# Optimization experiments

Hardware: AMD Instinct MI355X
Metric: run time of the kernel (lower is better)

The kernel has to match this reference:

```python
import jax, jax.numpy as jnp
import numpy as np

N, E, G = 100000, 1600000, 128
IN, HID, HEADS, EDIM, OUT = 16, 32, 4, 8, 4
HC = HEADS * HID


def _p(k, shape):
    return jax.random.normal(k, shape, jnp.float32) * 0.1


def setup_inputs():
    key = jax.random.key(0)
    ks = list(jax.random.split(key, 24))
    nxt = iter(ks)
    d = dict(
        x=jax.random.normal(next(nxt), (N, IN), jnp.float32),
        edge_index=jax.random.randint(next(nxt), (2, E), 0, N),
        edge_attr=jax.random.normal(next(nxt), (E, EDIM), jnp.float32),
        batch=jnp.sort(jax.random.randint(next(nxt), (N,), 0, G)),
    )
    # conv1: in=IN -> heads*hid
    d['wl1'] = _p(next(nxt), (IN, HC));  d['bl1'] = jnp.zeros((HC,), jnp.float32)
    d['wr1'] = _p(next(nxt), (IN, HC));  d['br1'] = jnp.zeros((HC,), jnp.float32)
    d['we1'] = _p(next(nxt), (EDIM, HC)); d['att1'] = _p(next(nxt), (HEADS, HID)); d['bc1'] = jnp.zeros((HC,), jnp.float32)
    # conv2: in=HC -> heads*hid
    d['wl2'] = _p(next(nxt), (HC, HC));  d['bl2'] = jnp.zeros((HC,), jnp.float32)
    d['wr2'] = _p(next(nxt), (HC, HC));  d['br2'] = jnp.zeros((HC,), jnp.float32)
    d['we2'] = _p(next(nxt), (EDIM, HC)); d['att2'] = _p(next(nxt), (HEADS, HID)); d['bc2'] = jnp.zeros((HC,), jnp.float32)
    # conv3: in=HC -> 1*hid (heads=1)
    d['wl3'] = _p(next(nxt), (HC, HID)); d['bl3'] = jnp.zeros((HID,), jnp.float32)
    d['wr3'] = _p(next(nxt), (HC, HID)); d['br3'] = jnp.zeros((HID,), jnp.float32)
    d['we3'] = _p(next(nxt), (EDIM, HID)); d['att3'] = _p(next(nxt), (1, HID)); d['bc3'] = jnp.zeros((HID,), jnp.float32)
    d['w_fc1'] = _p(next(nxt), (HID, 2 * HID)); d['b_fc1'] = jnp.zeros((2 * HID,), jnp.float32)
    d['w_fc2'] = _p(next(nxt), (2 * HID, OUT)); d['b_fc2'] = jnp.zeros((OUT,), jnp.float32)
    return d


def _gatv2(x, src, dst, eattr, wl, bl, wr, br, we, att, bias, n):
    # PyG GATv2Conv: e_ij = a^T . leaky_relu(Wl x_j + Wr x_i + We e_ij)
    H, C = att.shape
    xl = (x @ wl + bl).reshape(-1, H, C)  # source transform [N,H,C]
    xr = (x @ wr + br).reshape(-1, H, C)  # target transform [N,H,C]
    ea = (eattr @ we).reshape(-1, H, C)   # edge transform   [E,H,C]
    e = jax.nn.leaky_relu(xl[src] + xr[dst] + ea, 0.2)  # [E,H,C]
    logit = jnp.einsum('ehc,hc->eh', e, att)            # [E,H]
    m = jax.ops.segment_max(logit, dst, num_segments=n)
    p = jnp.exp(logit - m[dst])
    s = jax.ops.segment_sum(p, dst, num_segments=n)
    alpha = p / (s[dst] + 1e-16)                        # segment softmax per dst
    out = jax.ops.segment_sum(xl[src] * alpha[:, :, None], dst, num_segments=n)
    return out.reshape(n, H * C) + bias


def reference(x, edge_index, edge_attr, batch,
              wl1, bl1, wr1, br1, we1, att1, bc1,
              wl2, bl2, wr2, br2, we2, att2, bc2,
              wl3, bl3, wr3, br3, we3, att3, bc3,
              w_fc1, b_fc1, w_fc2, b_fc2):
    n = x.shape[0]
    src, dst = edge_index[0], edge_index[1]
    # add_self_loops=True with fill_value='mean' (mean of incoming edge_attr per node)
    ones_e = jnp.ones((src.shape[0],), x.dtype)
    cnt = jax.ops.segment_sum(ones_e, dst, num_segments=n)
    loop_attr = jax.ops.segment_sum(edge_attr, dst, num_segments=n) / jnp.maximum(cnt, 1.0)[:, None]
    ar = jnp.arange(n)
    src_a = jnp.concatenate([src, ar])
    dst_a = jnp.concatenate([dst, ar])
    ea = jnp.concatenate([edge_attr, loop_attr], axis=0)

    h = jax.nn.elu(_gatv2(x, src_a, dst_a, ea, wl1, bl1, wr1, br1, we1, att1, bc1, n))
    h = jax.nn.elu(_gatv2(h, src_a, dst_a, ea, wl2, bl2, wr2, br2, we2, att2, bc2, n))
    h = jax.nn.elu(_gatv2(h, src_a, dst_a, ea, wl3, bl3, wr3, br3, we3, att3, bc3, n))

    # global mean pool over graphs
    gs = jax.ops.segment_sum(h, batch, num_segments=G)
    gc = jax.ops.segment_sum(jnp.ones((n,), h.dtype), batch, num_segments=G)
    g = gs / jnp.maximum(gc, 1.0)[:, None]

    g = jax.nn.elu(g @ w_fc1 + b_fc1)
    return g @ w_fc2 + b_fc2
```

## Files before the change

### kernel.cpp

```cpp
#include <hip/hip_runtime.h>
#include <cstdint>
#include <type_traits>

constexpr int GNUM = 128;

typedef _Float16 h2 __attribute__((ext_vector_type(2)));
typedef _Float16 h4 __attribute__((ext_vector_type(4)));
typedef _Float16 h8 __attribute__((ext_vector_type(8)));
typedef float f4 __attribute__((ext_vector_type(4)));


__global__ __launch_bounds__(256) void hist_kernel(const int* __restrict__ dst,
                                                   int* __restrict__ cnt, int E) {
  int i = blockIdx.x * 256 + threadIdx.x;
  if (i < E) atomicAdd(&cnt[dst[i]], 1);
}

__global__ __launch_bounds__(256) void scan_part_kernel(const int* __restrict__ cnt,
                                                        int* __restrict__ bpart, int n) {
  __shared__ int red[256];
  int base = blockIdx.x * 512;
  int t = threadIdx.x;
  int s = 0;
  int i0 = base + t, i1 = base + 256 + t;
  if (i0 < n) s += cnt[i0] + 1;
  if (i1 < n) s += cnt[i1] + 1;
  red[t] = s;
  __syncthreads();
  for (int off = 128; off > 0; off >>= 1) {
    if (t < off) red[t] += red[t + off];
    __syncthreads();
  }
  if (t == 0) bpart[blockIdx.x] = red[0];
}

__global__ __launch_bounds__(1024) void scan_top_kernel(const int* __restrict__ bpart,
                                                        int* __restrict__ boff,
                                                        int* __restrict__ row_ptr,
                                                        int B, int n) {
  __shared__ int buf[1024];
  int t = threadIdx.x;
  buf[t] = (t < B) ? bpart[t] : 0;
  __syncthreads();
  for (int off = 1; off < 1024; off <<= 1) {
    int v = (t >= off) ? buf[t - off] : 0;
    __syncthreads();
    buf[t] += v;
    __syncthreads();
  }
  if (t < B) boff[t] = (t == 0) ? 0 : buf[t - 1];
  if (t == 0) row_ptr[n] = buf[1023];
}

__global__ __launch_bounds__(256) void scan_write_kernel(const int* __restrict__ cnt,
                                                         const int* __restrict__ boff,
                                                         int* __restrict__ row_ptr,
                                                         int* __restrict__ fill, int n) {
  __shared__ int red[256];
  int base = blockIdx.x * 512;
  int t = threadIdx.x;
  int i0 = base + 2 * t, i1 = base + 2 * t + 1;
  int v0 = (i0 < n) ? cnt[i0] + 1 : 0;
  int v1 = (i1 < n) ? cnt[i1] + 1 : 0;
  int val = v0 + v1;
  red[t] = val;
  __syncthreads();
  for (int off = 1; off < 256; off <<= 1) {
    int u = (t >= off) ? red[t - off] : 0;
    __syncthreads();
    red[t] += u;
    __syncthreads();
  }
  int o = boff[blockIdx.x] + red[t] - val;
  if (i0 < n) { row_ptr[i0] = o; fill[i0] = o; }
  if (i1 < n) { row_ptr[i1] = o + v0; fill[i1] = o + v0; }
}

__global__ __launch_bounds__(256) void scatter_kernel(const int* __restrict__ src,
                                                      const int* __restrict__ dst,
                                                      const float* __restrict__ ea,
                                                      int* __restrict__ fill,
                                                      int* __restrict__ csr_src,
                                                      _Float16* __restrict__ ea_csr, int E) {
  int i = blockIdx.x * 256 + threadIdx.x;
  if (i >= E) return;
  int d = dst[i];
  int p = atomicAdd(&fill[d], 1);
  csr_src[p] = src[i];
  float4 e0 = *(const float4*)&ea[(size_t)i * 8];
  float4 e1 = *(const float4*)&ea[(size_t)i * 8 + 4];
  h8 v;
  v[0] = (_Float16)e0.x; v[1] = (_Float16)e0.y; v[2] = (_Float16)e0.z; v[3] = (_Float16)e0.w;
  v[4] = (_Float16)e1.x; v[5] = (_Float16)e1.y; v[6] = (_Float16)e1.z; v[7] = (_Float16)e1.w;
  *(h8*)&ea_csr[(size_t)p * 8] = v;
}

__global__ __launch_bounds__(256) void selfloop_kernel(const int* __restrict__ row_ptr,
                                                       int* __restrict__ csr_src,
                                                       _Float16* __restrict__ ea_csr, int n) {
  int idx = blockIdx.x * 256 + threadIdx.x;
  int i = idx >> 3, c = idx & 7;
  if (i >= n) return;
  int s = row_ptr[i], e = row_ptr[i + 1] - 1;
  float a = 0.f;
  for (int j = s; j < e; j++) a += (float)ea_csr[(size_t)j * 8 + c];
  float inv = 1.f / fmaxf((float)(e - s), 1.f);
  ea_csr[(size_t)e * 8 + c] = (_Float16)(a * inv);
  if (c == 0) csr_src[e] = i;
}

__global__ __launch_bounds__(256) void pack_kernel(const float* __restrict__ w0,
                                                   _Float16* __restrict__ wp0,
                                                   const float* __restrict__ w1,
                                                   _Float16* __restrict__ wp1,
                                                   int Kreal, int Kpad, int NC) {
  const float* w = blockIdx.y ? w1 : w0;
  _Float16* wp = blockIdx.y ? wp1 : wp0;
  int KB = Kpad / 32;
  int total = (NC / 16) * KB * 64;
  int idx = blockIdx.x * 256 + threadIdx.x;
  if (idx >= total) return;
  int lane = idx & 63;
  int blk = idx >> 6;
  int nt = blk / KB, kb = blk % KB;
  int col = nt * 16 + (lane & 15);
  int krow = kb * 32 + (lane >> 4) * 8;
  h8 v;
#pragma unroll
  for (int j = 0; j < 8; j++)
    v[j] = (krow + j < Kreal) ? (_Float16)w[(size_t)(krow + j) * NC + col] : (_Float16)0.f;
  *(h8*)&wp[(size_t)idx * 8] = v;
}

__global__ __launch_bounds__(256) void cvt16_kernel(const float* __restrict__ x,
                                                    _Float16* __restrict__ x16, int total4) {
  int i = blockIdx.x * 256 + threadIdx.x;
  if (i >= total4) return;
  float4 v = ((const float4*)x)[i];
  h4 o;
  o[0] = (_Float16)v.x; o[1] = (_Float16)v.y; o[2] = (_Float16)v.z; o[3] = (_Float16)v.w;
  ((h4*)x16)[i] = o;
}


template <int K, int NCOLS>
__global__ __launch_bounds__(256) void k1m_kernel(const _Float16* __restrict__ x,
                                                  const _Float16* __restrict__ wp0,
                                                  const float* __restrict__ b0,
                                                  _Float16* __restrict__ out0,
                                                  const _Float16* __restrict__ wp1,
                                                  const float* __restrict__ b1,
                                                  _Float16* __restrict__ out1, int n) {
  constexpr int NT = NCOLS / 16, KB = K / 32;
  const _Float16* wp = blockIdx.y ? wp1 : wp0;
  const float* b = blockIdx.y ? b1 : b0;
  _Float16* out = blockIdx.y ? out1 : out0;

  int tid = threadIdx.x;
  int wave = tid >> 6, lane = tid & 63;
  int m = lane & 15, quad = lane >> 4;
  int node0 = blockIdx.x * 64 + wave * 16;

  h8 afrag[KB];
  int anode = node0 + m;
  if (anode < n) {
#pragma unroll
    for (int kb = 0; kb < KB; kb++)
      afrag[kb] = *(const h8*)&x[(size_t)anode * K + kb * 32 + quad * 8];
  } else {
#pragma unroll
    for (int kb = 0; kb < KB; kb++) afrag[kb] = (h8)(_Float16)0.f;
  }

  f4 acc[NT] = {};
#pragma unroll
  for (int nt = 0; nt < NT; nt++) {
#pragma unroll
    for (int kb = 0; kb < KB; kb++) {
      h8 bfrag = *(const h8*)&wp[((size_t)(nt * KB + kb) * 64 + lane) * 8];
      acc[nt] = __builtin_amdgcn_mfma_f32_16x16x32_f16(afrag[kb], bfrag, acc[nt], 0, 0, 0);
    }
  }

#pragma unroll
  for (int nt = 0; nt < NT; nt++) {
#pragma unroll
    for (int r = 0; r < 4; r++) {
      int row = node0 + quad * 4 + r;
      if (row < n) {
        int col = nt * 16 + m;
        out[(size_t)row * NCOLS + col] = (_Float16)(acc[nt][r] + b[col]);
      }
    }
  }
}

template <int NCOLS>
__global__ __launch_bounds__(256) void k1m16_kernel(const _Float16* __restrict__ x16,
                                                    const _Float16* __restrict__ wp0,
                                                    const float* __restrict__ b0,
                                                    _Float16* __restrict__ out0,
                                                    const _Float16* __restrict__ wp1,
                                                    const float* __restrict__ b1,
                                                    _Float16* __restrict__ out1, int n) {
  constexpr int NT = NCOLS / 16;
  const _Float16* wp = blockIdx.y ? wp1 : wp0;
  const float* b = blockIdx.y ? b1 : b0;
  _Float16* out = blockIdx.y ? out1 : out0;

  int tid = threadIdx.x;
  int wave = tid >> 6, lane = tid & 63;
  int m = lane & 15, quad = lane >> 4;
  int node0 = blockIdx.x * 64 + wave * 16;

  int anode = node0 + m;
  h8 afrag;
  if (anode < n && quad < 2)
    afrag = *(const h8*)&x16[(size_t)anode * 16 + quad * 8];
  else
    afrag = (h8)(_Float16)0.f;

  f4 acc[NT] = {};
#pragma unroll
  for (int nt = 0; nt < NT; nt++) {
    h8 bfrag = *(const h8*)&wp[((size_t)nt * 64 + lane) * 8];
    acc[nt] = __builtin_amdgcn_mfma_f32_16x16x32_f16(afrag, bfrag, acc[nt], 0, 0, 0);
  }

#pragma unroll
  for (int nt = 0; nt < NT; nt++) {
#pragma unroll
    for (int r = 0; r < 4; r++) {
      int row = node0 + quad * 4 + r;
      if (row < n) {
        int col = nt * 16 + m;
        out[(size_t)row * NCOLS + col] = (_Float16)(acc[nt][r] + b[col]);
      }
    }
  }
}

template <int H>
__global__ __launch_bounds__(128) void k2_kernel(
    const _Float16* __restrict__ xl, const _Float16* __restrict__ xr,
    const int* __restrict__ row_ptr, const int* __restrict__ csr_src,
    const _Float16* __restrict__ ea_csr, const float* __restrict__ we,
    const float* __restrict__ att, const float* __restrict__ bc,
    _Float16* __restrict__ out, int n) {
  constexpr int HC = H * 32;
  constexpr int NL = HC / 4;
  constexpr int NPB = 128 / NL;

  int tid = threadIdx.x;
  int ln = tid / NL, q = tid % NL;
  int c0 = 4 * q;
  int node = blockIdx.x * NPB + ln;
  if (node >= n) return;

  h2 w2[8][2];
#pragma unroll
  for (int k = 0; k < 8; k++) {
    float4 v = *(const float4*)&we[k * HC + c0];
    w2[k][0] = h2{(_Float16)v.x, (_Float16)v.y};
    w2[k][1] = h2{(_Float16)v.z, (_Float16)v.w};
  }
  const float LOG2E = 1.44269504088896f;
  float4 av = *(const float4*)&att[c0];
  h2 a0 = h2{(_Float16)(av.x * LOG2E), (_Float16)(av.y * LOG2E)};
  h2 a1 = h2{(_Float16)(av.z * LOG2E), (_Float16)(av.w * LOG2E)};
  h4 xrh = *(const h4*)&xr[(size_t)node * HC + c0];
  h2 xr0 = h2{xrh[0], xrh[1]}, xr1 = h2{xrh[2], xrh[3]};
  const h2 p2 = h2{(_Float16)0.2f, (_Float16)0.2f};

  float acc[4] = {0.f, 0.f, 0.f, 0.f};
  float s = 0.f;

  int start = row_ptr[node], end = row_ptr[node + 1];
  int len = end - start;
  int pairs = (len + 1) >> 1;

  int j1 = (start + 1 < end) ? start + 1 : start;
  float m1 = (start + 1 < end) ? 1.f : 0.f;
  int s0 = csr_src[start], s1 = csr_src[j1];
  h8 e0 = *(const h8*)&ea_csr[(size_t)start * 8];
  h8 e1 = *(const h8*)&ea_csr[(size_t)j1 * 8];
  h4 x0 = *(const h4*)&xl[(size_t)s0 * HC + c0];
  h4 x1 = *(const h4*)&xl[(size_t)s1 * HC + c0];

  for (int p = 0; p < pairs; p++) {
    int jn = start + 2 * (p + 1);
    int k0 = (jn < end) ? jn : start;
    int k1 = (jn + 1 < end) ? jn + 1 : k0;
    float nm1 = (jn + 1 < end) ? 1.f : 0.f;
    int ns0 = csr_src[k0], ns1 = csr_src[k1];
    h8 ne0 = *(const h8*)&ea_csr[(size_t)k0 * 8];
    h8 ne1 = *(const h8*)&ea_csr[(size_t)k1 * 8];

    h2 t00 = h2{x0[0], x0[1]} + xr0;
    h2 t01 = h2{x0[2], x0[3]} + xr1;
    h2 t10 = h2{x1[0], x1[1]} + xr0;
    h2 t11 = h2{x1[2], x1[3]} + xr1;
#pragma unroll
    for (int k = 0; k < 8; k++) {
      h2 ev0 = h2{e0[k], e0[k]};
      h2 ev1 = h2{e1[k], e1[k]};
      t00 += ev0 * w2[k][0];
      t01 += ev0 * w2[k][1];
      t10 += ev1 * w2[k][0];
      t11 += ev1 * w2[k][1];
    }
    t00 = __builtin_elementwise_max(t00, t00 * p2);
    t01 = __builtin_elementwise_max(t01, t01 * p2);
    t10 = __builtin_elementwise_max(t10, t10 * p2);
    t11 = __builtin_elementwise_max(t11, t11 * p2);
    h2 pd0 = t00 * a0 + t01 * a1;
    h2 pd1 = t10 * a0 + t11 * a1;
    float part0 = (float)pd0[0] + (float)pd0[1];
    float part1 = (float)pd1[0] + (float)pd1[1];

    h4 nx0 = *(const h4*)&xl[(size_t)ns0 * HC + c0];
    h4 nx1 = *(const h4*)&xl[(size_t)ns1 * HC + c0];

    part0 += __shfl_xor(part0, 1, 64);
    part1 += __shfl_xor(part1, 1, 64);
    part0 += __shfl_xor(part0, 2, 64);
    part1 += __shfl_xor(part1, 2, 64);
    part0 += __shfl_xor(part0, 4, 64);
    part1 += __shfl_xor(part1, 4, 64);
    float pe0 = __builtin_amdgcn_exp2f(part0);
    float pe1 = __builtin_amdgcn_exp2f(part1) * m1;
    s += pe0 + pe1;
#pragma unroll
    for (int i = 0; i < 4; i++)
      acc[i] += pe0 * (float)x0[i] + pe1 * (float)x1[i];

    s0 = ns0; s1 = ns1; e0 = ne0; e1 = ne1; x0 = nx0; x1 = nx1; m1 = nm1;
  }

  float inv = 1.f / (s + 1e-16f);
  h4 o;
#pragma unroll
  for (int i = 0; i < 4; i++) {
    float v = acc[i] * inv + bc[c0 + i];
    o[i] = (_Float16)(v > 0.f ? v : (__expf(v) - 1.f));
  }
  *(h4*)&out[(size_t)node * HC + c0] = o;
}


__global__ __launch_bounds__(256) void gbound_kernel(const int* __restrict__ batch,
                                                     int* __restrict__ gstart, int n) {
  int g = blockIdx.x * 256 + threadIdx.x;
  if (g > GNUM) return;
  int lo = 0, hi = n;
  while (lo < hi) {
    int mid = (lo + hi) >> 1;
    if (batch[mid] < g) lo = mid + 1; else hi = mid;
  }
  gstart[g] = lo;
}

__global__ __launch_bounds__(256) void pool2_kernel(const _Float16* __restrict__ h,
                                                    const int* __restrict__ gstart,
                                                    float* __restrict__ gmean) {
  __shared__ float red[256];
  int g = blockIdx.x;
  int t = threadIdx.x;
  int s = gstart[g], e = gstart[g + 1];
  int c = t & 31, rg = t >> 5;
  float acc = 0.f;
  for (int i = s + rg; i < e; i += 8) acc += (float)h[(size_t)i * 32 + c];
  red[t] = acc;
  __syncthreads();
  if (t < 128) red[t] += red[t + 128];
  __syncthreads();
  if (t < 64) red[t] += red[t + 64];
  __syncthreads();
  if (t < 32) {
    float v = red[t] + red[t + 32];
    gmean[g * 32 + t] = v / fmaxf((float)(e - s), 1.f);
  }
}

__global__ __launch_bounds__(64) void fc_kernel(const float* __restrict__ gmean,
                                                const float* __restrict__ w1,
                                                const float* __restrict__ b1,
                                                const float* __restrict__ w2,
                                                const float* __restrict__ b2,
                                                float* __restrict__ out) {
  __shared__ float g[32];
  __shared__ float a1[64];
  int gi = blockIdx.x;
  int t = threadIdx.x;
  if (t < 32) g[t] = gmean[gi * 32 + t];
  __syncthreads();
  float v = b1[t];
  for (int k = 0; k < 32; k++) v += g[k] * w1[k * 64 + t];
  a1[t] = v > 0.f ? v : (__expf(v) - 1.f);
  __syncthreads();
  if (t < 4) {
    float o = b2[t];
    for (int k = 0; k < 64; k++) o += a1[k] * w2[k * 4 + t];
    out[gi * 4 + t] = o;
  }
}


extern "C" void kernel_launch(void* const* d_in, const int* in_sizes, int n_in,
                              void* d_out, int out_size, void* d_ws, size_t ws_size,
                              hipStream_t stream) {
  const float* x     = (const float*)d_in[0];
  const int*   ei    = (const int*)d_in[1];
  const float* eattr = (const float*)d_in[2];
  const int*   batch = (const int*)d_in[3];
  const float *wl1 = (const float*)d_in[4],  *bl1 = (const float*)d_in[5];
  const float *wr1 = (const float*)d_in[6],  *br1 = (const float*)d_in[7];
  const float *we1 = (const float*)d_in[8],  *at1 = (const float*)d_in[9];
  const float *bc1 = (const float*)d_in[10];
  const float *wl2 = (const float*)d_in[11], *bl2 = (const float*)d_in[12];
  const float *wr2 = (const float*)d_in[13], *br2 = (const float*)d_in[14];
  const float *we2 = (const float*)d_in[15], *at2 = (const float*)d_in[16];
  const float *bc2 = (const float*)d_in[17];
  const float *wl3 = (const float*)d_in[18], *bl3 = (const float*)d_in[19];
  const float *wr3 = (const float*)d_in[20], *br3 = (const float*)d_in[21];
  const float *we3 = (const float*)d_in[22], *at3 = (const float*)d_in[23];
  const float *bc3 = (const float*)d_in[24];
  const float *wf1 = (const float*)d_in[25], *bf1 = (const float*)d_in[26];
  const float *wf2 = (const float*)d_in[27], *bf2 = (const float*)d_in[28];

  int N = in_sizes[0] / 16;
  int E = in_sizes[1] / 2;
  const int* srcp = ei;
  const int* dstp = ei + E;
  int EA = E + N;
  int NB = (N + 511) / 512;

  char* wsb = (char*)d_ws;
  size_t off = 0;
  auto alloc = [&](size_t bytes) -> char* {
    char* p = wsb + off;
    off += (bytes + 255) & ~(size_t)255;
    return p;
  };
  int*       cnt     = (int*)alloc((size_t)N * 4);
  int*       row_ptr = (int*)alloc((size_t)(N + 1) * 4);
  int*       fill    = (int*)alloc((size_t)N * 4);
  int*       bpart   = (int*)alloc((size_t)1024 * 4);
  int*       boff    = (int*)alloc((size_t)1024 * 4);
  int*       csr_src = (int*)alloc((size_t)EA * 4);
  _Float16*  ea_csr  = (_Float16*)alloc((size_t)EA * 8 * 2);
  _Float16*  xl      = (_Float16*)alloc((size_t)N * 128 * 2);
  _Float16*  xr      = (_Float16*)alloc((size_t)N * 128 * 2);
  _Float16*  h16     = (_Float16*)alloc((size_t)N * 128 * 2);
  _Float16*  h3      = (_Float16*)alloc((size_t)N * 32 * 2);
  _Float16*  x16     = (_Float16*)alloc((size_t)N * 16 * 2);
  float*     gmean   = (float*)alloc((size_t)GNUM * 32 * 4);
  int*       gstart  = (int*)alloc((size_t)(GNUM + 1) * 4);
  _Float16*  wp1l    = (_Float16*)alloc((size_t)32 * 128 * 2);
  _Float16*  wp1r    = (_Float16*)alloc((size_t)32 * 128 * 2);
  _Float16*  wp2l    = (_Float16*)alloc((size_t)128 * 128 * 2);
  _Float16*  wp2r    = (_Float16*)alloc((size_t)128 * 128 * 2);
  _Float16*  wp3l    = (_Float16*)alloc((size_t)128 * 32 * 2);
  _Float16*  wp3r    = (_Float16*)alloc((size_t)128 * 32 * 2);

  hipMemsetAsync(cnt, 0, (size_t)N * 4, stream);

  hist_kernel<<<(E + 255) / 256, 256, 0, stream>>>(dstp, cnt, E);
  scan_part_kernel<<<NB, 256, 0, stream>>>(cnt, bpart, N);
  scan_top_kernel<<<1, 1024, 0, stream>>>(bpart, boff, row_ptr, NB, N);
  scan_write_kernel<<<NB, 256, 0, stream>>>(cnt, boff, row_ptr, fill, N);
  scatter_kernel<<<(E + 255) / 256, 256, 0, stream>>>(srcp, dstp, eattr, fill, csr_src, ea_csr, E);
  selfloop_kernel<<<(N * 8 + 255) / 256, 256, 0, stream>>>(row_ptr, csr_src, ea_csr, N);
  gbound_kernel<<<1, 256, 0, stream>>>(batch, gstart, N);
  cvt16_kernel<<<(N * 4 + 255) / 256, 256, 0, stream>>>(x, x16, N * 4);
  pack_kernel<<<dim3(2, 2), 256, 0, stream>>>(wl1, wp1l, wr1, wp1r, 16, 32, 128);
  pack_kernel<<<dim3(8, 2), 256, 0, stream>>>(wl2, wp2l, wr2, wp2r, 128, 128, 128);
  pack_kernel<<<dim3(2, 2), 256, 0, stream>>>(wl3, wp3l, wr3, wp3r, 128, 128, 32);

  k1m16_kernel<128><<<dim3((N + 63) / 64, 2), 256, 0, stream>>>(
      x16, wp1l, bl1, xl, wp1r, br1, xr, N);
  k2_kernel<4><<<(N + 3) / 4, 128, 0, stream>>>(xl, xr, row_ptr, csr_src, ea_csr,
                                                we1, at1, bc1, h16, N);
  k1m_kernel<128, 128><<<dim3((N + 63) / 64, 2), 256, 0, stream>>>(
      h16, wp2l, bl2, xl, wp2r, br2, xr, N);
  k2_kernel<4><<<(N + 3) / 4, 128, 0, stream>>>(xl, xr, row_ptr, csr_src, ea_csr,
                                                we2, at2, bc2, h16, N);
  k1m_kernel<128, 32><<<dim3((N + 63) / 64, 2), 256, 0, stream>>>(
      h16, wp3l, bl3, xl, wp3r, br3, xr, N);
  k2_kernel<1><<<(N + 15) / 16, 128, 0, stream>>>(xl, xr, row_ptr, csr_src, ea_csr,
                                                  we3, at3, bc3, h3, N);

  pool2_kernel<<<GNUM, 256, 0, stream>>>(h3, gstart, gmean);
  fc_kernel<<<GNUM, 64, 0, stream>>>(gmean, wf1, bf1, wf2, bf2, (float*)d_out);
}
```

Baseline: 717.0 us.

## Fuse small setup and tail kernels to cut launch count

Several small launches are folded into their neighbours. The graph-boundary binary search moves into the scan_top kernel, and the three weight-pack launches become one. The x-to-fp16 conversion now happens inside the first matmul's operand load, and the pool and FC kernels are merged into one. This removes per-launch overhead and one intermediate fp16 buffer. An unroll-2 pragma is also added to the k2 edge loop, which may raise register pressure.

Measured after the change: 684.6 us. 1.05x faster.

```diff
diff --git a/kernel.cpp b/kernel.cpp
--- a/kernel.cpp
+++ b/kernel.cpp
@@ -37,6 +37,8 @@
 __global__ __launch_bounds__(1024) void scan_top_kernel(const int* __restrict__ bpart,
                                                         int* __restrict__ boff,
                                                         int* __restrict__ row_ptr,
+                                                        const int* __restrict__ batch,
+                                                        int* __restrict__ gstart,
                                                         int B, int n) {
   __shared__ int buf[1024];
   int t = threadIdx.x;
@@ -50,6 +52,14 @@
   }
   if (t < B) boff[t] = (t == 0) ? 0 : buf[t - 1];
   if (t == 0) row_ptr[n] = buf[1023];
+  if (t <= GNUM) {
+    int lo = 0, hi = n;
+    while (lo < hi) {
+      int mid = (lo + hi) >> 1;
+      if (batch[mid] < t) lo = mid + 1; else hi = mid;
+    }
+    gstart[t] = lo;
+  }
 }
 
 __global__ __launch_bounds__(256) void scan_write_kernel(const int* __restrict__ cnt,
@@ -109,13 +119,23 @@
   if (c == 0) csr_src[e] = i;
 }
 
-__global__ __launch_bounds__(256) void pack_kernel(const float* __restrict__ w0,
-                                                   _Float16* __restrict__ wp0,
-                                                   const float* __restrict__ w1,
-                                                   _Float16* __restrict__ wp1,
-                                                   int Kreal, int Kpad, int NC) {
-  const float* w = blockIdx.y ? w1 : w0;
-  _Float16* wp = blockIdx.y ? wp1 : wp0;
+__global__ __launch_bounds__(256) void pack_all_kernel(
+    const float* __restrict__ wl1, _Float16* __restrict__ p1l,
+    const float* __restrict__ wr1, _Float16* __restrict__ p1r,
+    const float* __restrict__ wl2, _Float16* __restrict__ p2l,
+    const float* __restrict__ wr2, _Float16* __restrict__ p2r,
+    const float* __restrict__ wl3, _Float16* __restrict__ p3l,
+    const float* __restrict__ wr3, _Float16* __restrict__ p3r) {
+  int y = blockIdx.y;
+  const float* w; _Float16* wp; int Kreal, Kpad, NC;
+  switch (y) {
+    case 0: w = wl1; wp = p1l; Kreal = 16;  Kpad = 32;  NC = 128; break;
+    case 1: w = wr1; wp = p1r; Kreal = 16;  Kpad = 32;  NC = 128; break;
+    case 2: w = wl2; wp = p2l; Kreal = 128; Kpad = 128; NC = 128; break;
+    case 3: w = wr2; wp = p2r; Kreal = 128; Kpad = 128; NC = 128; break;
+    case 4: w = wl3; wp = p3l; Kreal = 128; Kpad = 128; NC = 32;  break;
+    default: w = wr3; wp = p3r; Kreal = 128; Kpad = 128; NC = 32; break;
+  }
   int KB = Kpad / 32;
   int total = (NC / 16) * KB * 64;
   int idx = blockIdx.x * 256 + threadIdx.x;
@@ -130,16 +150,6 @@
   for (int j = 0; j < 8; j++)
     v[j] = (krow + j < Kreal) ? (_Float16)w[(size_t)(krow + j) * NC + col] : (_Float16)0.f;
   *(h8*)&wp[(size_t)idx * 8] = v;
-}
-
-__global__ __launch_bounds__(256) void cvt16_kernel(const float* __restrict__ x,
-                                                    _Float16* __restrict__ x16, int total4) {
-  int i = blockIdx.x * 256 + threadIdx.x;
-  if (i >= total4) return;
-  float4 v = ((const float4*)x)[i];
-  h4 o;
-  o[0] = (_Float16)v.x; o[1] = (_Float16)v.y; o[2] = (_Float16)v.z; o[3] = (_Float16)v.w;
-  ((h4*)x16)[i] = o;
 }
 
 
@@ -196,7 +206,7 @@
 }
 
 template <int NCOLS>
-__global__ __launch_bounds__(256) void k1m16_kernel(const _Float16* __restrict__ x16,
+__global__ __launch_bounds__(256) void k1m16_kernel(const float* __restrict__ x,
                                                     const _Float16* __restrict__ wp0,
                                                     const float* __restrict__ b0,
                                                     _Float16* __restrict__ out0,
@@ -214,11 +224,15 @@
   int node0 = blockIdx.x * 64 + wave * 16;
 
   int anode = node0 + m;
-  h8 afrag;
-  if (anode < n && quad < 2)
-    afrag = *(const h8*)&x16[(size_t)anode * 16 + quad * 8];
-  else
-    afrag = (h8)(_Float16)0.f;
+  h8 afrag = (h8)(_Float16)0.f;
+  if (anode < n && quad < 2) {
+    float4 v0 = *(const float4*)&x[(size_t)anode * 16 + quad * 8];
+    float4 v1 = *(const float4*)&x[(size_t)anode * 16 + quad * 8 + 4];
+    afrag[0] = (_Float16)v0.x; afrag[1] = (_Float16)v0.y;
+    afrag[2] = (_Float16)v0.z; afrag[3] = (_Float16)v0.w;
+    afrag[4] = (_Float16)v1.x; afrag[5] = (_Float16)v1.y;
+    afrag[6] = (_Float16)v1.z; afrag[7] = (_Float16)v1.w;
+  }
 
   f4 acc[NT] = {};
 #pragma unroll
@@ -287,6 +301,7 @@
   h4 x0 = *(const h4*)&xl[(size_t)s0 * HC + c0];
   h4 x1 = *(const h4*)&xl[(size_t)s1 * HC + c0];
 
+#pragma unroll 2
   for (int p = 0; p < pairs; p++) {
     int jn = start + 2 * (p + 1);
     int k0 = (jn < end) ? jn : start;
@@ -347,26 +362,19 @@
   *(h4*)&out[(size_t)node * HC + c0] = o;
 }
 
-
-__global__ __launch_bounds__(256) void gbound_kernel(const int* __restrict__ batch,
-                                                     int* __restrict__ gstart, int n) {
-  int g = blockIdx.x * 256 + threadIdx.x;
-  if (g > GNUM) return;
-  int lo = 0, hi = n;
-  while (lo < hi) {
-    int mid = (lo + hi) >> 1;
-    if (batch[mid] < g) lo = mid + 1; else hi = mid;
-  }
-  gstart[g] = lo;
-}
-
-__global__ __launch_bounds__(256) void pool2_kernel(const _Float16* __restrict__ h,
-                                                    const int* __restrict__ gstart,
-                                                    float* __restrict__ gmean) {
+__global__ __launch_bounds__(256) void poolfc_kernel(const _Float16* __restrict__ h,
+                                                     const int* __restrict__ gstart,
+                                                     const float* __restrict__ w1,
+                                                     const float* __restrict__ b1,
+                                                     const float* __restrict__ w2,
+                                                     const float* __restrict__ b2,
+                                                     float* __restrict__ out) {
   __shared__ float red[256];
-  int g = blockIdx.x;
+  __shared__ float g[32];
+  __shared__ float a1[64];
+  int gi = blockIdx.x;
   int t = threadIdx.x;
-  int s = gstart[g], e = gstart[g + 1];
+  int s = gstart[gi], e = gstart[gi + 1];
   int c = t & 31, rg = t >> 5;
   float acc = 0.f;
   for (int i = s + rg; i < e; i += 8) acc += (float)h[(size_t)i * 32 + c];
@@ -376,27 +384,13 @@
   __syncthreads();
   if (t < 64) red[t] += red[t + 64];
   __syncthreads();
-  if (t < 32) {
-    float v = red[t] + red[t + 32];
-    gmean[g * 32 + t] = v / fmaxf((float)(e - s), 1.f);
-  }
-}
-
-__global__ __launch_bounds__(64) void fc_kernel(const float* __restrict__ gmean,
-                                                const float* __restrict__ w1,
-                                                const float* __restrict__ b1,
-                                                const float* __restrict__ w2,
-                                                const float* __restrict__ b2,
-                                                float* __restrict__ out) {
-  __shared__ float g[32];
-  __shared__ float a1[64];
-  int gi = blockIdx.x;
-  int t = threadIdx.x;
-  if (t < 32) g[t] = gmean[gi * 32 + t];
-  __syncthreads();
-  float v = b1[t];
-  for (int k = 0; k < 32; k++) v += g[k] * w1[k * 64 + t];
-  a1[t] = v > 0.f ? v : (__expf(v) - 1.f);
+  if (t < 32) g[t] = (red[t] + red[t + 32]) / fmaxf((float)(e - s), 1.f);
+  __syncthreads();
+  if (t < 64) {
+    float v = b1[t];
+    for (int k = 0; k < 32; k++) v += g[k] * w1[k * 64 + t];
+    a1[t] = v > 0.f ? v : (__expf(v) - 1.f);
+  }
   __syncthreads();
   if (t < 4) {
     float o = b2[t];
@@ -453,8 +447,6 @@
   _Float16*  xr      = (_Float16*)alloc((size_t)N * 128 * 2);
   _Float16*  h16     = (_Float16*)alloc((size_t)N * 128 * 2);
   _Float16*  h3      = (_Float16*)alloc((size_t)N * 32 * 2);
-  _Float16*  x16     = (_Float16*)alloc((size_t)N * 16 * 2);
-  float*     gmean   = (float*)alloc((size_t)GNUM * 32 * 4);
   int*       gstart  = (int*)alloc((size_t)(GNUM + 1) * 4);
   _Float16*  wp1l    = (_Float16*)alloc((size_t)32 * 128 * 2);
   _Float16*  wp1r    = (_Float16*)alloc((size_t)32 * 128 * 2);
@@ -467,18 +459,16 @@
 
   hist_kernel<<<(E + 255) / 256, 256, 0, stream>>>(dstp, cnt, E);
   scan_part_kernel<<<NB, 256, 0, stream>>>(cnt, bpart, N);
-  scan_top_kernel<<<1, 1024, 0, stream>>>(bpart, boff, row_ptr, NB, N);
+  scan_top_kernel<<<1, 1024, 0, stream>>>(bpart, boff, row_ptr, batch, gstart, NB, N);
   scan_write_kernel<<<NB, 256, 0, stream>>>(cnt, boff, row_ptr, fill, N);
   scatter_kernel<<<(E + 255) / 256, 256, 0, stream>>>(srcp, dstp, eattr, fill, csr_src, ea_csr, E);
   selfloop_kernel<<<(N * 8 + 255) / 256, 256, 0, stream>>>(row_ptr, csr_src, ea_csr, N);
-  gbound_kernel<<<1, 256, 0, stream>>>(batch, gstart, N);
-  cvt16_kernel<<<(N * 4 + 255) / 256, 256, 0, stream>>>(x, x16, N * 4);
-  pack_kernel<<<dim3(2, 2), 256, 0, stream>>>(wl1, wp1l, wr1, wp1r, 16, 32, 128);
-  pack_kernel<<<dim3(8, 2), 256, 0, stream>>>(wl2, wp2l, wr2, wp2r, 128, 128, 128);
-  pack_kernel<<<dim3(2, 2), 256, 0, stream>>>(wl3, wp3l, wr3, wp3r, 128, 128, 32);
+  pack_all_kernel<<<dim3(8, 6), 256, 0, stream>>>(wl1, wp1l, wr1, wp1r,
+                                                  wl2, wp2l, wr2, wp2r,
+                                                  wl3, wp3l, wr3, wp3r);
 
   k1m16_kernel<128><<<dim3((N + 63) / 64, 2), 256, 0, stream>>>(
-      x16, wp1l, bl1, xl, wp1r, br1, xr, N);
+      x, wp1l, bl1, xl, wp1r, br1, xr, N);
   k2_kernel<4><<<(N + 3) / 4, 128, 0, stream>>>(xl, xr, row_ptr, csr_src, ea_csr,
                                                 we1, at1, bc1, h16, N);
   k1m_kernel<128, 128><<<dim3((N + 63) / 64, 2), 256, 0, stream>>>(
@@ -490,6 +480,5 @@
   k2_kernel<1><<<(N + 15) / 16, 128, 0, stream>>>(xl, xr, row_ptr, csr_src, ea_csr,
                                                   we3, at3, bc3, h3, N);
 
-  pool2_kernel<<<GNUM, 256, 0, stream>>>(h3, gstart, gmean);
-  fc_kernel<<<GNUM, 64, 0, stream>>>(gmean, wf1, bf1, wf2, bf2, (float*)d_out);
-}
+  poolfc_kernel<<<GNUM, 256, 0, stream>>>(h3, gstart, wf1, bf1, wf2, bf2, (float*)d_out);
+}
```
